# Kernel optimization log

Measured on AMD Instinct MI355X. Metric: run time of the kernel, lower is better.

## Reference

```python
import jax, jax.numpy as jnp
import numpy as np

A_CONST = 0.1
B_CONST = 0.2
C_CONST = 0.8

INPUT_SIZE = 1024
HIDDEN_SIZE = 2048
BATCH = 32768
SIGMA = 0.02


def acti_func(x, a, b, c):
    # piecewise: a*(1 - x/b) for x<=b ; 0 for b<x<c ; a*(x-c)/(1-c) for x>=c
    low = -a * x / b + a
    high = a * x / (1.0 - c) + a * c / (c - 1.0)
    return jnp.where(x <= b, low, jnp.where(x >= c, high, jnp.zeros_like(x)))


def setup_inputs() -> dict:
    key = jax.random.key(0)
    ks = jax.random.split(key, 4)
    x = jax.random.normal(ks[0], (BATCH, INPUT_SIZE), dtype=jnp.float32)
    W0 = jax.random.normal(ks[1], (INPUT_SIZE, HIDDEN_SIZE), dtype=jnp.float32) * SIGMA
    b0 = jnp.zeros((HIDDEN_SIZE,), dtype=jnp.float32)
    W1 = jax.random.normal(ks[2], (HIDDEN_SIZE, HIDDEN_SIZE), dtype=jnp.float32) * SIGMA
    b1 = jnp.zeros((HIDDEN_SIZE,), dtype=jnp.float32)
    W2 = jax.random.normal(ks[3], (HIDDEN_SIZE, 1), dtype=jnp.float32) * SIGMA
    b2 = jnp.zeros((1,), dtype=jnp.float32)
    return {"x": x, "W0": W0, "b0": b0, "W1": W1, "b1": b1, "W2": W2, "b2": b2}


def reference(x, W0, b0, W1, b1, W2, b2):
    h = jax.nn.elu(x @ W0 + b0)
    h = jax.nn.elu(h @ W1 + b1)
    out = jax.nn.sigmoid(h @ W2 + b2)  # [B, 1]
    alpha = acti_func(out, A_CONST, B_CONST, C_CONST)
    return out, alpha
```

## Files before the change

### kernel.cpp

```cpp
#include <hip/hip_runtime.h>
#include <hip/hip_bf16.h>
#include <stdint.h>

typedef unsigned short u16;
typedef __bf16 bf16x8 __attribute__((ext_vector_type(8)));
typedef float floatx4 __attribute__((ext_vector_type(4)));

__device__ __forceinline__ u16 f2bf(float f) {
  union { float f; unsigned u; } c; c.f = f;
  unsigned r = c.u + 0x7fffu + ((c.u >> 16) & 1u);
  return (u16)(r >> 16);
}

__device__ __forceinline__ void load_lds16(const void* g, void* l) {
  __builtin_amdgcn_global_load_lds(
      (const __attribute__((address_space(1))) void*)g,
      (__attribute__((address_space(3))) void*)l,
      16, 0, 0);
}

__global__ __launch_bounds__(256) void preamble(
    const float* __restrict__ x, const float* __restrict__ W0,
    const float* __restrict__ W1,
    u16* __restrict__ Xb, u16* __restrict__ Wt0, u16* __restrict__ Wt1,
    float* __restrict__ z)
{
  __shared__ float tile[32][33];
  const int bid = blockIdx.x;
  const int t = threadIdx.x;

  if (bid < 32768) {
    int i = bid * 256 + t;
    float4 f = ((const float4*)x)[i];
    ushort4 u;
    u.x = f2bf(f.x); u.y = f2bf(f.y); u.z = f2bf(f.z); u.w = f2bf(f.w);
    ((ushort4*)Xb)[i] = u;
  } else if (bid < 32768 + 2048) {
    int tb = bid - 32768;
    int bx = (tb & 63) * 32, by = (tb >> 6) * 32;
    int tx = t & 31, ty = t >> 5;
    #pragma unroll
    for (int i = 0; i < 32; i += 8)
      tile[ty + i][tx] = W0[(size_t)(by + ty + i) * 2048 + bx + tx];
    __syncthreads();
    #pragma unroll
    for (int i = 0; i < 32; i += 8)
      Wt0[(size_t)(bx + ty + i) * 1024 + by + tx] = f2bf(tile[tx][ty + i]);
  } else if (bid < 32768 + 2048 + 4096) {
    int tb = bid - (32768 + 2048);
    int bx = (tb & 63) * 32, by = (tb >> 6) * 32;
    int tx = t & 31, ty = t >> 5;
    #pragma unroll
    for (int i = 0; i < 32; i += 8)
      tile[ty + i][tx] = W1[(size_t)(by + ty + i) * 2048 + bx + tx];
    __syncthreads();
    #pragma unroll
    for (int i = 0; i < 32; i += 8)
      Wt1[(size_t)(bx + ty + i) * 2048 + by + tx] = f2bf(tile[tx][ty + i]);
  } else {
    int tb = bid - (32768 + 2048 + 4096);
    ((float4*)z)[tb * 256 + t] = (float4){0.f, 0.f, 0.f, 0.f};
  }
}

template<bool FUSE_HEAD>
__global__ __launch_bounds__(256) void gemm_bt_fused(
    const u16* __restrict__ A,
    const u16* __restrict__ Bt,
    const float* __restrict__ bias,
    u16* __restrict__ C,
    const float* __restrict__ W2,
    float* __restrict__ z,
    int M, int N, int K)
{
  __shared__ u16 As[128 * 64];
  __shared__ u16 Bs[128 * 64];

  const int t = threadIdx.x;
  const int w = t >> 6;
  const int l = t & 63;
  const int wm = w >> 1;
  const int wn = w & 1;
  const int lm = l & 15;
  const int q  = l >> 4;

  const int n0 = blockIdx.x * 128;
  const int m0 = blockIdx.y * 128;

  floatx4 acc[4][4];
  #pragma unroll
  for (int i = 0; i < 4; ++i)
    #pragma unroll
    for (int j = 0; j < 4; ++j)
      acc[i][j] = (floatx4){0.f, 0.f, 0.f, 0.f};

  const int rowoff = t >> 3;
  const int lc8 = ((t & 7) ^ (rowoff & 7)) * 8;
  const u16* Ap[4];
  const u16* Bp[4];
  #pragma unroll
  for (int k = 0; k < 4; ++k) {
    Ap[k] = A  + (size_t)(m0 + k * 32 + rowoff) * K + lc8;
    Bp[k] = Bt + (size_t)(n0 + k * 32 + rowoff) * K + lc8;
  }
  const int ldsoff = t * 8;

  const int sw0 = ((0 * 4 + q) ^ (lm & 7)) * 8;
  const int sw1 = ((1 * 4 + q) ^ (lm & 7)) * 8;

  for (int k0 = 0; k0 < K; k0 += 64) {
    __syncthreads();
    #pragma unroll
    for (int k = 0; k < 4; ++k) {
      load_lds16(Ap[k] + k0, &As[k * 2048 + ldsoff]);
      load_lds16(Bp[k] + k0, &Bs[k * 2048 + ldsoff]);
    }
    __syncthreads();

    {
      bf16x8 af[4], bfr[4];
      #pragma unroll
      for (int i = 0; i < 4; ++i)
        af[i] = *(const bf16x8*)(As + (wm * 64 + i * 16 + lm) * 64 + sw0);
      #pragma unroll
      for (int j = 0; j < 4; ++j)
        bfr[j] = *(const bf16x8*)(Bs + (wn * 64 + j * 16 + lm) * 64 + sw0);
      #pragma unroll
      for (int i = 0; i < 4; ++i)
        #pragma unroll
        for (int j = 0; j < 4; ++j)
          acc[i][j] = __builtin_amdgcn_mfma_f32_16x16x32_bf16(af[i], bfr[j], acc[i][j], 0, 0, 0);
    }
    {
      bf16x8 af[4], bfr[4];
      #pragma unroll
      for (int i = 0; i < 4; ++i)
        af[i] = *(const bf16x8*)(As + (wm * 64 + i * 16 + lm) * 64 + sw1);
      #pragma unroll
      for (int j = 0; j < 4; ++j)
        bfr[j] = *(const bf16x8*)(Bs + (wn * 64 + j * 16 + lm) * 64 + sw1);
      #pragma unroll
      for (int i = 0; i < 4; ++i)
        #pragma unroll
        for (int j = 0; j < 4; ++j)
          acc[i][j] = __builtin_amdgcn_mfma_f32_16x16x32_bf16(af[i], bfr[j], acc[i][j], 0, 0, 0);
    }
  }

  float bv[4];
  #pragma unroll
  for (int j = 0; j < 4; ++j) bv[j] = bias[n0 + wn * 64 + j * 16 + lm];

  if (!FUSE_HEAD) {
    #pragma unroll
    for (int i = 0; i < 4; ++i) {
      #pragma unroll
      for (int r = 0; r < 4; ++r) {
        int grow = m0 + wm * 64 + i * 16 + q * 4 + r;
        size_t base = (size_t)grow * N + n0 + wn * 64 + lm;
        #pragma unroll
        for (int j = 0; j < 4; ++j) {
          float v = acc[i][j][r] + bv[j];
          v = v > 0.f ? v : (__expf(v) - 1.f);
          C[base + j * 16] = f2bf(v);
        }
      }
    }
  } else {
    float w2v[4];
    #pragma unroll
    for (int j = 0; j < 4; ++j) w2v[j] = W2[n0 + wn * 64 + j * 16 + lm];
    #pragma unroll
    for (int i = 0; i < 4; ++i) {
      #pragma unroll
      for (int r = 0; r < 4; ++r) {
        float p = 0.f;
        #pragma unroll
        for (int j = 0; j < 4; ++j) {
          float v = acc[i][j][r] + bv[j];
          v = v > 0.f ? v : (__expf(v) - 1.f);
          p += v * w2v[j];
        }
        p += __shfl_xor(p, 1);
        p += __shfl_xor(p, 2);
        p += __shfl_xor(p, 4);
        p += __shfl_xor(p, 8);
        if (lm == 0) atomicAdd(&z[m0 + wm * 64 + i * 16 + q * 4 + r], p);
      }
    }
  }
}

__global__ __launch_bounds__(256) void sigmoid_alpha(
    const float* __restrict__ z, const float* __restrict__ b2,
    float* __restrict__ out, int B)
{
  int i = blockIdx.x * blockDim.x + threadIdx.x;
  if (i >= B) return;
  float o = 1.f / (1.f + expf(-(z[i] + b2[0])));
  float alpha;
  if (o <= 0.2f)      alpha = 0.1f - 0.5f * o;
  else if (o >= 0.8f) alpha = 0.5f * o - 0.4f;
  else                alpha = 0.f;
  out[i] = o;
  out[B + i] = alpha;
}

extern "C" void kernel_launch(void* const* d_in, const int* in_sizes, int n_in,
                              void* d_out, int out_size, void* d_ws, size_t ws_size,
                              hipStream_t stream) {
  const int BATCH = 32768, IN = 1024, HID = 2048;

  const float* x  = (const float*)d_in[0];
  const float* W0 = (const float*)d_in[1];
  const float* b0 = (const float*)d_in[2];
  const float* W1 = (const float*)d_in[3];
  const float* b1 = (const float*)d_in[4];
  const float* W2 = (const float*)d_in[5];
  const float* b2 = (const float*)d_in[6];
  float* out = (float*)d_out;

  char* ws = (char*)d_ws;
  u16* Xb   = (u16*)(ws);
  u16* Wt0  = (u16*)(ws + (size_t)67108864);
  u16* Wt1  = (u16*)(ws + (size_t)71303168);
  u16* h0   = (u16*)(ws + (size_t)79691776);
  float* z  = (float*)(ws + (size_t)213909504);

  preamble<<<32768 + 2048 + 4096 + 32, 256, 0, stream>>>(x, W0, W1, Xb, Wt0, Wt1, z);
  gemm_bt_fused<false><<<dim3(HID / 128, BATCH / 128), 256, 0, stream>>>(
      Xb, Wt0, b0, h0, nullptr, nullptr, BATCH, HID, IN);
  gemm_bt_fused<true><<<dim3(HID / 128, BATCH / 128), 256, 0, stream>>>(
      h0, Wt1, b1, nullptr, W2, z, BATCH, HID, HID);
  sigmoid_alpha<<<BATCH / 256, 256, 0, stream>>>(z, b2, out, BATCH);
}
```

Before: 662.6 us.

## Swizzle GEMM tile order for XCD L2 locality and fuse sigmoid head via completion counter

Remaps the flat block index so that blocks landing on the same XCD cover a compact 4x4 group of output tiles. This is meant to improve L2 reuse of the A and B panels. It also removes the separate sigmoid/alpha kernel: a per-row-tile atomic counter lets the last finishing block compute the outputs. This adds atomics and fences at the end of GEMM2 and relies on the counter zeroing done in the preamble.

```diff
diff --git a/kernel.cpp b/kernel.cpp
--- a/kernel.cpp
+++ b/kernel.cpp
@@ -23,7 +23,7 @@
     const float* __restrict__ x, const float* __restrict__ W0,
     const float* __restrict__ W1,
     u16* __restrict__ Xb, u16* __restrict__ Wt0, u16* __restrict__ Wt1,
-    float* __restrict__ z)
+    float* __restrict__ z, int* __restrict__ zc)
 {
   __shared__ float tile[32][33];
   const int bid = blockIdx.x;
@@ -59,8 +59,19 @@
       Wt1[(size_t)(bx + ty + i) * 2048 + by + tx] = f2bf(tile[tx][ty + i]);
   } else {
     int tb = bid - (32768 + 2048 + 4096);
-    ((float4*)z)[tb * 256 + t] = (float4){0.f, 0.f, 0.f, 0.f};
-  }
+    int i = tb * 256 + t;
+    if (i < 8192)            ((float4*)z)[i] = (float4){0.f, 0.f, 0.f, 0.f};
+    else if (i < 8192 + 64)  ((int4*)zc)[i - 8192] = (int4){0, 0, 0, 0};
+  }
+}
+
+__device__ __forceinline__ void swizzle_mn(int flat, int& m0, int& n0) {
+  int x = flat & 7;
+  int j = (flat >> 3) & 15;
+  int k = flat >> 7;
+  int s = k * 8 + x;
+  m0 = ((s >> 2) * 4 + (j >> 2)) * 128;
+  n0 = ((s & 3) * 4 + (j & 3)) * 128;
 }
 
 template<bool FUSE_HEAD>
@@ -71,10 +82,14 @@
     u16* __restrict__ C,
     const float* __restrict__ W2,
     float* __restrict__ z,
+    int* __restrict__ zc,
+    const float* __restrict__ b2,
+    float* __restrict__ outp,
     int M, int N, int K)
 {
   __shared__ u16 As[128 * 64];
   __shared__ u16 Bs[128 * 64];
+  __shared__ int lastflag;
 
   const int t = threadIdx.x;
   const int w = t >> 6;
@@ -84,8 +99,8 @@
   const int lm = l & 15;
   const int q  = l >> 4;
 
-  const int n0 = blockIdx.x * 128;
-  const int m0 = blockIdx.y * 128;
+  int m0, n0;
+  swizzle_mn(blockIdx.x, m0, n0);
 
   floatx4 acc[4][4];
   #pragma unroll
@@ -188,22 +203,27 @@
         if (lm == 0) atomicAdd(&z[m0 + wm * 64 + i * 16 + q * 4 + r], p);
       }
     }
-  }
-}
-
-__global__ __launch_bounds__(256) void sigmoid_alpha(
-    const float* __restrict__ z, const float* __restrict__ b2,
-    float* __restrict__ out, int B)
-{
-  int i = blockIdx.x * blockDim.x + threadIdx.x;
-  if (i >= B) return;
-  float o = 1.f / (1.f + expf(-(z[i] + b2[0])));
-  float alpha;
-  if (o <= 0.2f)      alpha = 0.1f - 0.5f * o;
-  else if (o >= 0.8f) alpha = 0.5f * o - 0.4f;
-  else                alpha = 0.f;
-  out[i] = o;
-  out[B + i] = alpha;
+    __syncthreads();
+    if (t == 0) {
+      __threadfence();
+      lastflag = (atomicAdd(&zc[m0 >> 7], 1) == 15);
+    }
+    __syncthreads();
+    if (lastflag) {
+      __threadfence();
+      if (t < 128) {
+        int row = m0 + t;
+        float zz = atomicAdd(&z[row], 0.f);
+        float o = 1.f / (1.f + expf(-(zz + b2[0])));
+        float alpha;
+        if (o <= 0.2f)      alpha = 0.1f - 0.5f * o;
+        else if (o >= 0.8f) alpha = 0.5f * o - 0.4f;
+        else                alpha = 0.f;
+        outp[row] = o;
+        outp[M + row] = alpha;
+      }
+    }
+  }
 }
 
 extern "C" void kernel_launch(void* const* d_in, const int* in_sizes, int n_in,
@@ -226,11 +246,11 @@
   u16* Wt1  = (u16*)(ws + (size_t)71303168);
   u16* h0   = (u16*)(ws + (size_t)79691776);
   float* z  = (float*)(ws + (size_t)213909504);
-
-  preamble<<<32768 + 2048 + 4096 + 32, 256, 0, stream>>>(x, W0, W1, Xb, Wt0, Wt1, z);
-  gemm_bt_fused<false><<<dim3(HID / 128, BATCH / 128), 256, 0, stream>>>(
-      Xb, Wt0, b0, h0, nullptr, nullptr, BATCH, HID, IN);
-  gemm_bt_fused<true><<<dim3(HID / 128, BATCH / 128), 256, 0, stream>>>(
-      h0, Wt1, b1, nullptr, W2, z, BATCH, HID, HID);
-  sigmoid_alpha<<<BATCH / 256, 256, 0, stream>>>(z, b2, out, BATCH);
-}
+  int* zc   = (int*)(ws + (size_t)213909504 + 131072);
+
+  preamble<<<32768 + 2048 + 4096 + 33, 256, 0, stream>>>(x, W0, W1, Xb, Wt0, Wt1, z, zc);
+  gemm_bt_fused<false><<<4096, 256, 0, stream>>>(
+      Xb, Wt0, b0, h0, nullptr, nullptr, nullptr, nullptr, nullptr, BATCH, HID, IN);
+  gemm_bt_fused<true><<<4096, 256, 0, stream>>>(
+      h0, Wt1, b1, nullptr, W2, z, zc, b2, out, BATCH, HID, HID);
+}
```

After: 888.0 us. 34.0% more time.
